# Kernel optimization log

Measured on AMD Instinct MI355X. Metric: run time of the kernel, lower is better.

## Reference

```python
import jax, jax.numpy as jnp
import numpy as np

N, T, F, H = 4096, 365, 16, 20  # nodes, timesteps (int(4383/12)), input feats, hidden
N_CLASSES = 1
STD = 0.02


def setup_inputs() -> dict:
    key = jax.random.key(0)
    ks = jax.random.split(key, 14)
    rn = lambda k, shp: (STD * jax.random.normal(k, shp)).astype(jnp.float32)
    # Keras LSTM default init: glorot kernel/orthogonal recurrent; normal(0.02) is a
    # faithful stand-in for random weights (the TF code builds the LSTM inside call).
    lstm_bias = jnp.zeros((4 * H,), jnp.float32).at[H:2 * H].set(1.0)  # unit_forget_bias
    return {
        "inputs": jax.random.normal(ks[0], (N, T, F), jnp.float32),
        "A": jax.random.uniform(ks[1], (N, N), jnp.float32),
        "lstm_kernel": rn(ks[2], (F, 4 * H)),
        "lstm_rec": rn(ks[3], (H, 4 * H)),
        "lstm_bias": lstm_bias,
        "W_graph_h": rn(ks[4], (H, H)),
        "b_graph_h": jnp.zeros((H,), jnp.float32),
        "W_graph_c": rn(ks[5], (H, H)),
        "b_graph_c": jnp.zeros((H,), jnp.float32),
        "W_h_cur": rn(ks[6], (H, H)),
        "W_h_prev": rn(ks[7], (H, H)),
        "b_h": jnp.zeros((H,), jnp.float32),
        "W_c_cur": rn(ks[8], (H, H)),
        "W_c_prev": rn(ks[9], (H, H)),
        "b_c": jnp.zeros((H,), jnp.float32),
        "W_out": rn(ks[10], (H, N_CLASSES)),
        "b_out": jnp.zeros((N_CLASSES,), jnp.float32),
    }


def _lstm_step(x, h, c, Wk, Wr, b):
    # Keras LSTM cell: gates in order i, f, g(cand), o.
    z = x @ Wk + h @ Wr + b
    i, f, g, o = jnp.split(z, 4, axis=-1)
    c = jax.nn.sigmoid(f) * c + jax.nn.sigmoid(i) * jnp.tanh(g)
    h = jax.nn.sigmoid(o) * jnp.tanh(c)
    return h, c


def reference(inputs, A, lstm_kernel, lstm_rec, lstm_bias,
              W_graph_h, b_graph_h, W_graph_c, b_graph_c,
              W_h_cur, W_h_prev, b_h, W_c_cur, W_c_prev, b_c,
              W_out, b_out):
    n, hid = inputs.shape[0], W_graph_h.shape[0]
    xs = jnp.swapaxes(inputs, 0, 1)  # [T, N, F]

    # lstm(inputs): run full sequence from zero state -> final (h, c)
    def warm(carry, x_t):
        h, c = _lstm_step(x_t, carry[0], carry[1], lstm_kernel, lstm_rec, lstm_bias)
        return (h, c), None
    z0 = jnp.zeros((n, hid), inputs.dtype)
    (h0, c0), _ = jax.lax.scan(warm, (z0, z0), xs)

    # graph-gated recurrence over t = 1 .. T-1
    def step(carry, x_t):
        h_prev, c_prev = carry
        h_graph = jnp.tanh(A @ (h_prev @ W_graph_h + b_graph_h))
        c_graph = jnp.tanh(A @ (c_prev @ W_graph_c + b_graph_c))
        h_cur, c_cur = _lstm_step(x_t, h_prev, c_prev, lstm_kernel, lstm_rec, lstm_bias)
        h_upd = jax.nn.sigmoid(h_cur @ W_h_cur + h_graph @ W_h_prev + b_h)
        c_upd = jax.nn.sigmoid(c_cur @ W_c_cur + c_graph @ W_c_prev + b_c)
        return (h_upd, c_upd), h_upd

    _, outs = jax.lax.scan(step, (h0, c0), xs[1:])  # [T-1, N, H]
    out = outs.reshape(-1, hid)                      # [(T-1)*N, H]
    return out @ W_out + b_out                       # [(T-1)*N, 1]
```

## Files before the change

### kernel.cpp

```cpp
#include <hip/hip_runtime.h>


#define NN   4096
#define TT   365
#define FF   16
#define HH   20
#define G4   80
#define RPB  16
#define NBLK 256
#define NTHR 512
#define NWV  8
#define XRG  42
#define KSPL 512
#define NFRG 16

typedef float f4 __attribute__((ext_vector_type(4)));
typedef short s8v __attribute__((ext_vector_type(8)));

__device__ __attribute__((aligned(16))) unsigned short g_X[(size_t)TT * XRG * NN];
__device__ unsigned g_flag[NBLK];

struct __align__(16) Smem {
  float WkT[G4][FF];
  float WrT[G4][HH];
  float WghT[HH][HH]; float WgcT[HH][HH];
  float WhcT[HH][HH]; float WhpT[HH][HH];
  float WccT[HH][HH]; float WcpT[HH][HH];
  float Wout[HH];
  float bias[G4];
  float bgh[HH]; float bgc[HH]; float bhv[HH]; float bcv[HH];
  float bout; float pad0[3];
  float hprev[RPB][HH]; float cprev[RPB][HH];
  float hcur[RPB][HH];  float ccur[RPB][HH];
  float hg[RPB][HH];    float cg[RPB][HH];
  float cen[2 * HH];
  float SA[RPB];
  float sAp[32][16];
  float part[NWV][3][16][17];
};

__device__ inline float sigm(float x) { return 1.f / (1.f + __expf(-x)); }
__device__ inline float tanh_f(float x) { return 2.f / (1.f + __expf(-2.f * x)) - 1.f; }

__device__ inline unsigned short f2bf(float f) {
  unsigned u = __float_as_uint(f);
  u = u + 0x7FFFu + ((u >> 16) & 1u);
  return (unsigned short)(u >> 16);
}
__device__ inline float bf2f(unsigned short u) {
  return __uint_as_float(((unsigned)u) << 16);
}

__device__ inline void load_x(const float* __restrict__ inputs, int nb0, int t,
                              int tid, f4* x) {
  const float* xr = inputs + ((size_t)(nb0 + (tid & 15)) * TT + t) * FF;
  x[0] = *(const f4*)(xr);
  x[1] = *(const f4*)(xr + 4);
  x[2] = *(const f4*)(xr + 8);
  x[3] = *(const f4*)(xr + 12);
}

__device__ inline void lstm_cells_x(Smem& sm, const f4* x, int tid) {
  const int n = tid & 15;
  const f4* hpr = (const f4*)sm.hprev[n];
  const f4 hp0 = hpr[0], hp1 = hpr[1], hp2 = hpr[2], hp3 = hpr[3], hp4 = hpr[4];
  for (int idx = tid; idx < RPB * HH; idx += NTHR) {
    const int h = idx >> 4;
    float z[4];
#pragma unroll
    for (int g = 0; g < 4; g++) {
      const int col = g * HH + h;
      const f4* wk = (const f4*)sm.WkT[col];
      f4 acc = x[0] * wk[0] + x[1] * wk[1] + x[2] * wk[2] + x[3] * wk[3];
      const f4* wr = (const f4*)sm.WrT[col];
      acc += hp0 * wr[0] + hp1 * wr[1] + hp2 * wr[2] + hp3 * wr[3] + hp4 * wr[4];
      z[g] = sm.bias[col] + acc[0] + acc[1] + acc[2] + acc[3];
    }
    const float co = sm.cprev[n][h];
    const float cn = sigm(z[1]) * co + sigm(z[0]) * tanh_f(z[2]);
    const float hn = sigm(z[3]) * tanh_f(cn);
    sm.hcur[n][h] = hn;
    sm.ccur[n][h] = cn;
  }
}

__device__ inline void produce_X(Smem& sm, int gen, int nb0, int tid) {
  for (int idx = tid; idx < 8 * 2 * HH; idx += NTHR) {
    const int p = idx & 7, j = idx >> 3;
    const int n0 = p * 2;
    const f4* w; float b0; const f4* s0; const f4* s1;
    if (j < HH) {
      w = (const f4*)sm.WghT[j];     b0 = sm.bgh[j];
      s0 = (const f4*)sm.hprev[n0];  s1 = (const f4*)sm.hprev[n0 + 1];
    } else {
      w = (const f4*)sm.WgcT[j-HH];  b0 = sm.bgc[j - HH];
      s0 = (const f4*)sm.cprev[n0];  s1 = (const f4*)sm.cprev[n0 + 1];
    }
    const f4 w0 = w[0], w1 = w[1], w2 = w[2], w3 = w[3], w4 = w[4];
    f4 a0 = s0[0]*w0 + s0[1]*w1 + s0[2]*w2 + s0[3]*w3 + s0[4]*w4;
    f4 a1 = s1[0]*w0 + s1[1]*w1 + s1[2]*w2 + s1[3]*w3 + s1[4]*w4;
    const float c0 = sm.cen[j];
    const unsigned short lo = f2bf(b0 + a0[0] + a0[1] + a0[2] + a0[3] - c0);
    const unsigned short hi = f2bf(b0 + a1[0] + a1[1] + a1[2] + a1[3] - c0);
    const unsigned v = (unsigned)lo | ((unsigned)hi << 16);
    unsigned* dst = (unsigned*)(g_X + (((size_t)gen * XRG + j) << 12) + (unsigned)(nb0 + n0));
    __hip_atomic_store(dst, v, __ATOMIC_RELAXED, __HIP_MEMORY_SCOPE_AGENT);
  }
}

__device__ inline void publish(int tid, unsigned gen) {
  asm volatile("s_waitcnt vmcnt(0)" ::: "memory");
  __syncthreads();
  if (tid == 0)
    __hip_atomic_store(&g_flag[blockIdx.x], gen,
                       __ATOMIC_RELAXED, __HIP_MEMORY_SCOPE_AGENT);
}

__global__ void bar_init() {
  const int i = threadIdx.x;
  if (i < NBLK)
    __hip_atomic_store(&g_flag[i], 0u, __ATOMIC_RELAXED, __HIP_MEMORY_SCOPE_AGENT);
}

__global__ void __launch_bounds__(NTHR, 2)
gg_kernel(const float* __restrict__ inputs, const float* __restrict__ Ag,
          const float* __restrict__ Wk, const float* __restrict__ Wr, const float* __restrict__ bls,
          const float* __restrict__ Wgh, const float* __restrict__ bgh,
          const float* __restrict__ Wgc, const float* __restrict__ bgc,
          const float* __restrict__ Whc, const float* __restrict__ Whp, const float* __restrict__ bh,
          const float* __restrict__ Wcc, const float* __restrict__ Wcp, const float* __restrict__ bc,
          const float* __restrict__ Wo, const float* __restrict__ bo,
          float* __restrict__ out) {
  __shared__ Smem sm;
  const int tid  = threadIdx.x;
  const int nb0  = blockIdx.x * RPB;
  const int lane = tid & 63;
  const int wv   = tid >> 6;
  const int li   = lane & 15;
  const int quad = lane >> 4;

  for (int i = tid; i < FF * G4; i += NTHR) sm.WkT[i % G4][i / G4] = Wk[i];
  for (int i = tid; i < HH * G4; i += NTHR) sm.WrT[i % G4][i / G4] = Wr[i];
  for (int i = tid; i < HH * HH; i += NTHR) {
    const int r = i / HH, c = i % HH;
    sm.WghT[c][r] = Wgh[i]; sm.WgcT[c][r] = Wgc[i];
    sm.WhcT[c][r] = Whc[i]; sm.WhpT[c][r] = Whp[i];
    sm.WccT[c][r] = Wcc[i]; sm.WcpT[c][r] = Wcp[i];
  }
  for (int i = tid; i < G4; i += NTHR) sm.bias[i] = bls[i];
  if (tid < HH) { sm.bgh[tid] = bgh[tid]; sm.bgc[tid] = bgc[tid]; sm.bhv[tid] = bh[tid]; sm.bcv[tid] = bc[tid]; sm.Wout[tid] = Wo[tid]; }
  if (tid == 0) sm.bout = bo[0];
  for (int i = tid; i < RPB * HH; i += NTHR) { (&sm.hprev[0][0])[i] = 0.f; (&sm.cprev[0][0])[i] = 0.f; }
  __syncthreads();

  if (tid < 2 * HH) {
    const int j = tid;
    float s = 0.f;
    if (j < HH) { for (int h = 0; h < HH; h++) s += sm.WghT[j][h]; s = sm.bgh[j] + 0.5f * s; }
    else        { for (int h = 0; h < HH; h++) s += sm.WgcT[j - HH][h]; s = sm.bgc[j - HH] + 0.5f * s; }
    sm.cen[j] = s;
  }

  s8v afrag[NFRG];
  {
    const float* Arow = Ag + (size_t)(nb0 + li) * NN + (size_t)(wv * KSPL + quad * 8);
    double ds = 0.0;
#pragma unroll
    for (int i = 0; i < NFRG; i++) {
      const f4 v0 = *(const f4*)(Arow + i * 32);
      const f4 v1 = *(const f4*)(Arow + i * 32 + 4);
      s8v tb;
      tb[0] = (short)f2bf(v0[0]); tb[1] = (short)f2bf(v0[1]);
      tb[2] = (short)f2bf(v0[2]); tb[3] = (short)f2bf(v0[3]);
      tb[4] = (short)f2bf(v1[0]); tb[5] = (short)f2bf(v1[1]);
      tb[6] = (short)f2bf(v1[2]); tb[7] = (short)f2bf(v1[3]);
      afrag[i] = tb;
#pragma unroll
      for (int e = 0; e < 8; e++) ds += (double)bf2f((unsigned short)tb[e]);
    }
    sm.sAp[wv * 4 + quad][li] = (float)ds;
  }
  __syncthreads();
  if (tid < RPB) {
    float s = 0.f;
#pragma unroll
    for (int g = 0; g < 32; g++) s += sm.sAp[g][tid];
    sm.SA[tid] = s;
  }

  f4 xa[4], xb[4];
  load_x(inputs, nb0, 0, tid, xa);
  for (int t = 0; t < TT; t++) {
    if (t + 1 < TT) load_x(inputs, nb0, t + 1, tid, xb);
    __syncthreads();
    lstm_cells_x(sm, xa, tid);
    __syncthreads();
    for (int i = tid; i < RPB * HH; i += NTHR) {
      (&sm.hprev[0][0])[i] = (&sm.hcur[0][0])[i];
      (&sm.cprev[0][0])[i] = (&sm.ccur[0][0])[i];
    }
    xa[0] = xb[0]; xa[1] = xb[1]; xa[2] = xb[2]; xa[3] = xb[3];
  }
  __syncthreads();

  produce_X(sm, 1, nb0, tid);
  publish(tid, 1u);
  load_x(inputs, nb0, 1, tid, xa);
  lstm_cells_x(sm, xa, tid);

  for (int t = 1; t < TT; t++) {
    if (t + 1 < TT) load_x(inputs, nb0, t + 1, tid, xa);

    for (;;) {
      int ok = 1;
      if (lane < 32)
        ok = (__hip_atomic_load(&g_flag[(wv << 5) + lane], __ATOMIC_RELAXED,
                                __HIP_MEMORY_SCOPE_AGENT) >= (unsigned)t);
      if (__all(ok)) break;
      __builtin_amdgcn_s_sleep(1);
    }
    asm volatile("" ::: "memory");
    __builtin_amdgcn_sched_barrier(0);

    const unsigned short* Xt = g_X + (((size_t)t * XRG) << 12)
                             + (size_t)(wv * KSPL + quad * 8);
#pragma unroll
    for (int c = 0; c < 3; c++) {
      int row = c * 16 + li;
      if (row >= 2 * HH) row = 2 * HH;
      const unsigned short* Xrow = Xt + ((size_t)row << 12);
      f4 a0 = {0.f, 0.f, 0.f, 0.f}, a1 = a0, a2 = a0, a3 = a0;
#pragma unroll
      for (int i = 0; i < NFRG; i += 4) {
        a0 = __builtin_amdgcn_mfma_f32_16x16x32_bf16(afrag[i + 0], *(const s8v*)(Xrow + (i + 0) * 32), a0, 0, 0, 0);
        a1 = __builtin_amdgcn_mfma_f32_16x16x32_bf16(afrag[i + 1], *(const s8v*)(Xrow + (i + 1) * 32), a1, 0, 0, 0);
        a2 = __builtin_amdgcn_mfma_f32_16x16x32_bf16(afrag[i + 2], *(const s8v*)(Xrow + (i + 2) * 32), a2, 0, 0, 0);
        a3 = __builtin_amdgcn_mfma_f32_16x16x32_bf16(afrag[i + 3], *(const s8v*)(Xrow + (i + 3) * 32), a3, 0, 0, 0);
      }
      const f4 ac = (a0 + a1) + (a2 + a3);
#pragma unroll
      for (int r = 0; r < 4; r++) sm.part[wv][c][quad * 4 + r][li] = ac[r];
    }
    __syncthreads();

#pragma unroll
    for (int p = 0; p < 2; p++) {
      const int idx = tid + NTHR * p;
      if (idx < 768) {
        const int c = idx >> 8, rc = idx & 255, r = rc >> 4, col = rc & 15;
        const int gc = c * 16 + col;
        if (gc < 2 * HH) {
          float s = 0.f;
#pragma unroll
          for (int w = 0; w < NWV; w++) s += sm.part[w][c][r][col];
          const float v = s + sm.SA[r] * sm.cen[gc];
          const float tv = tanh_f(v);
          if (gc < HH) sm.hg[r][gc] = tv; else sm.cg[r][gc - HH] = tv;
        }
      }
    }
    __syncthreads();

    for (int idx = tid; idx < 2 * RPB * HH; idx += NTHR) {
      int q = idx; int cpath = 0;
      if (q >= RPB * HH) { q -= RPB * HH; cpath = 1; }
      const int n = q & 15, h = q >> 4;
      const f4* cur = (const f4*)(cpath ? sm.ccur[n] : sm.hcur[n]);
      const f4* gr2 = (const f4*)(cpath ? sm.cg[n] : sm.hg[n]);
      const f4* w1  = (const f4*)(cpath ? sm.WccT[h] : sm.WhcT[h]);
      const f4* w2  = (const f4*)(cpath ? sm.WcpT[h] : sm.WhpT[h]);
      f4 acc = cur[0]*w1[0] + cur[1]*w1[1] + cur[2]*w1[2] + cur[3]*w1[3] + cur[4]*w1[4];
      acc   += gr2[0]*w2[0] + gr2[1]*w2[1] + gr2[2]*w2[2] + gr2[3]*w2[3] + gr2[4]*w2[4];
      const float b0 = cpath ? sm.bcv[h] : sm.bhv[h];
      const float v = sigm(b0 + acc[0] + acc[1] + acc[2] + acc[3]);
      if (cpath) sm.cprev[n][h] = v; else sm.hprev[n][h] = v;
    }
    __syncthreads();

    if (t < TT - 1) {
      produce_X(sm, t + 1, nb0, tid);
      publish(tid, (unsigned)(t + 1));
    }

    if (tid < RPB) {
      float acc = sm.bout;
#pragma unroll
      for (int h2 = 0; h2 < HH; h2++) acc += sm.hprev[tid][h2] * sm.Wout[h2];
      out[(size_t)(t - 1) * NN + nb0 + tid] = acc;
    }

    if (t < TT - 1) {
      lstm_cells_x(sm, xa, tid);
    }
  }
}

extern "C" void kernel_launch(void* const* d_in, const int* in_sizes, int n_in,
                              void* d_out, int out_size, void* d_ws, size_t ws_size,
                              hipStream_t stream) {
  (void)in_sizes; (void)n_in; (void)out_size; (void)d_ws; (void)ws_size;
  const float* inputs = (const float*)d_in[0];
  const float* Ag     = (const float*)d_in[1];
  const float* Wk     = (const float*)d_in[2];
  const float* Wr     = (const float*)d_in[3];
  const float* bls    = (const float*)d_in[4];
  const float* Wgh    = (const float*)d_in[5];
  const float* bgh    = (const float*)d_in[6];
  const float* Wgc    = (const float*)d_in[7];
  const float* bgc    = (const float*)d_in[8];
  const float* Whc    = (const float*)d_in[9];
  const float* Whp    = (const float*)d_in[10];
  const float* bh     = (const float*)d_in[11];
  const float* Wcc    = (const float*)d_in[12];
  const float* Wcp    = (const float*)d_in[13];
  const float* bc     = (const float*)d_in[14];
  const float* Wo     = (const float*)d_in[15];
  const float* bo     = (const float*)d_in[16];
  float* out = (float*)d_out;

  bar_init<<<dim3(1), dim3(256), 0, stream>>>();

  void* args[] = { (void*)&inputs, (void*)&Ag, (void*)&Wk, (void*)&Wr, (void*)&bls,
                   (void*)&Wgh, (void*)&bgh, (void*)&Wgc, (void*)&bgc,
                   (void*)&Whc, (void*)&Whp, (void*)&bh,
                   (void*)&Wcc, (void*)&Wcp, (void*)&bc,
                   (void*)&Wo, (void*)&bo, (void*)&out };
  hipError_t err = hipLaunchCooperativeKernel((void*)gg_kernel, dim3(NBLK), dim3(NTHR),
                                              args, 0, stream);
  if (err != hipSuccess) {
    (void)hipGetLastError();
    gg_kernel<<<dim3(NBLK), dim3(NTHR), 0, stream>>>(inputs, Ag, Wk, Wr, bls,
                                                     Wgh, bgh, Wgc, bgc,
                                                     Whc, Whp, bh, Wcc, Wcp, bc,
                                                     Wo, bo, out);
  }
}
```

Before: 5.590 ms.

## Replace per-block flag barrier with sentinel-value polling on exchanged data

```diff
diff --git a/kernel.cpp b/kernel.cpp
--- a/kernel.cpp
+++ b/kernel.cpp
@@ -16,9 +16,9 @@
 
 typedef float f4 __attribute__((ext_vector_type(4)));
 typedef short s8v __attribute__((ext_vector_type(8)));
+typedef unsigned u4v __attribute__((ext_vector_type(4)));
 
 __device__ __attribute__((aligned(16))) unsigned short g_X[(size_t)TT * XRG * NN];
-__device__ unsigned g_flag[NBLK];
 
 struct __align__(16) Smem {
   float WkT[G4][FF];
@@ -108,20 +108,6 @@
   }
 }
 
-__device__ inline void publish(int tid, unsigned gen) {
-  asm volatile("s_waitcnt vmcnt(0)" ::: "memory");
-  __syncthreads();
-  if (tid == 0)
-    __hip_atomic_store(&g_flag[blockIdx.x], gen,
-                       __ATOMIC_RELAXED, __HIP_MEMORY_SCOPE_AGENT);
-}
-
-__global__ void bar_init() {
-  const int i = threadIdx.x;
-  if (i < NBLK)
-    __hip_atomic_store(&g_flag[i], 0u, __ATOMIC_RELAXED, __HIP_MEMORY_SCOPE_AGENT);
-}
-
 __global__ void __launch_bounds__(NTHR, 2)
 gg_kernel(const float* __restrict__ inputs, const float* __restrict__ Ag,
           const float* __restrict__ Wk, const float* __restrict__ Wr, const float* __restrict__ bls,
@@ -204,38 +190,47 @@
   __syncthreads();
 
   produce_X(sm, 1, nb0, tid);
-  publish(tid, 1u);
   load_x(inputs, nb0, 1, tid, xa);
   lstm_cells_x(sm, xa, tid);
 
   for (int t = 1; t < TT; t++) {
     if (t + 1 < TT) load_x(inputs, nb0, t + 1, tid, xa);
 
-    for (;;) {
-      int ok = 1;
-      if (lane < 32)
-        ok = (__hip_atomic_load(&g_flag[(wv << 5) + lane], __ATOMIC_RELAXED,
-                                __HIP_MEMORY_SCOPE_AGENT) >= (unsigned)t);
-      if (__all(ok)) break;
-      __builtin_amdgcn_s_sleep(1);
-    }
-    asm volatile("" ::: "memory");
-    __builtin_amdgcn_sched_barrier(0);
-
     const unsigned short* Xt = g_X + (((size_t)t * XRG) << 12)
                              + (size_t)(wv * KSPL + quad * 8);
 #pragma unroll
     for (int c = 0; c < 3; c++) {
       int row = c * 16 + li;
-      if (row >= 2 * HH) row = 2 * HH;
+      if (row >= 2 * HH) row = 0;
       const unsigned short* Xrow = Xt + ((size_t)row << 12);
+      u4v fr[NFRG];
+#pragma unroll
+      for (int i = 0; i < NFRG; i++) fr[i] = *(const u4v*)(Xrow + i * 32);
+      for (;;) {
+        unsigned anybad = 0;
+#pragma unroll
+        for (int i = 0; i < NFRG; i++) {
+          const unsigned b = (fr[i][0] == 0xFFFFFFFFu) | (fr[i][1] == 0xFFFFFFFFu)
+                           | (fr[i][2] == 0xFFFFFFFFu) | (fr[i][3] == 0xFFFFFFFFu);
+          anybad |= b;
+          if (b) {
+            const unsigned* p = (const unsigned*)(Xrow + i * 32);
+            fr[i][0] = __hip_atomic_load(p + 0, __ATOMIC_RELAXED, __HIP_MEMORY_SCOPE_AGENT);
+            fr[i][1] = __hip_atomic_load(p + 1, __ATOMIC_RELAXED, __HIP_MEMORY_SCOPE_AGENT);
+            fr[i][2] = __hip_atomic_load(p + 2, __ATOMIC_RELAXED, __HIP_MEMORY_SCOPE_AGENT);
+            fr[i][3] = __hip_atomic_load(p + 3, __ATOMIC_RELAXED, __HIP_MEMORY_SCOPE_AGENT);
+          }
+        }
+        if (!__any(anybad)) break;
+        __builtin_amdgcn_s_sleep(1);
+      }
       f4 a0 = {0.f, 0.f, 0.f, 0.f}, a1 = a0, a2 = a0, a3 = a0;
 #pragma unroll
       for (int i = 0; i < NFRG; i += 4) {
-        a0 = __builtin_amdgcn_mfma_f32_16x16x32_bf16(afrag[i + 0], *(const s8v*)(Xrow + (i + 0) * 32), a0, 0, 0, 0);
-        a1 = __builtin_amdgcn_mfma_f32_16x16x32_bf16(afrag[i + 1], *(const s8v*)(Xrow + (i + 1) * 32), a1, 0, 0, 0);
-        a2 = __builtin_amdgcn_mfma_f32_16x16x32_bf16(afrag[i + 2], *(const s8v*)(Xrow + (i + 2) * 32), a2, 0, 0, 0);
-        a3 = __builtin_amdgcn_mfma_f32_16x16x32_bf16(afrag[i + 3], *(const s8v*)(Xrow + (i + 3) * 32), a3, 0, 0, 0);
+        a0 = __builtin_amdgcn_mfma_f32_16x16x32_bf16(afrag[i + 0], __builtin_bit_cast(s8v, fr[i + 0]), a0, 0, 0, 0);
+        a1 = __builtin_amdgcn_mfma_f32_16x16x32_bf16(afrag[i + 1], __builtin_bit_cast(s8v, fr[i + 1]), a1, 0, 0, 0);
+        a2 = __builtin_amdgcn_mfma_f32_16x16x32_bf16(afrag[i + 2], __builtin_bit_cast(s8v, fr[i + 2]), a2, 0, 0, 0);
+        a3 = __builtin_amdgcn_mfma_f32_16x16x32_bf16(afrag[i + 3], __builtin_bit_cast(s8v, fr[i + 3]), a3, 0, 0, 0);
       }
       const f4 ac = (a0 + a1) + (a2 + a3);
 #pragma unroll
@@ -277,10 +272,7 @@
     }
     __syncthreads();
 
-    if (t < TT - 1) {
-      produce_X(sm, t + 1, nb0, tid);
-      publish(tid, (unsigned)(t + 1));
-    }
+    if (t < TT - 1) produce_X(sm, t + 1, nb0, tid);
 
     if (tid < RPB) {
       float acc = sm.bout;
@@ -318,7 +310,9 @@
   const float* bo     = (const float*)d_in[16];
   float* out = (float*)d_out;
 
-  bar_init<<<dim3(1), dim3(256), 0, stream>>>();
+  void* xptr = nullptr;
+  if (hipGetSymbolAddress(&xptr, HIP_SYMBOL(g_X)) == hipSuccess && xptr)
+    hipMemsetAsync(xptr, 0xFF, sizeof(g_X), stream);
 
   void* args[] = { (void*)&inputs, (void*)&Ag, (void*)&Wk, (void*)&Wr, (void*)&bls,
                    (void*)&Wgh, (void*)&bgh, (void*)&Wgc, (void*)&bgc,
```

Result: slower. 8.719 ms (+56.0%).
